# Kernel optimization log

Hardware: AMD Instinct MI355X
Metric: run time of the kernel (lower is better)

The kernel has to match this reference:

```python
import jax, jax.numpy as jnp
from jax import lax
import numpy as np

C, C_MID, K_ENC, K_UP, SCALE = 128, 64, 3, 5, 2
B, H, W = 4, 48, 48
BN_EPS = 1e-3  # ultralytics Conv BN eps
EPS = 1e-6


def setup_inputs() -> dict:
    key = jax.random.key(0)
    ks = jax.random.split(key, 12)
    n_enc = (SCALE * K_UP) ** 2  # 100
    return {
        "x": jax.random.uniform(ks[0], (B, C, H, W), dtype=jnp.float32),
        "comp_w": jax.random.normal(ks[1], (C_MID, C, 1, 1), dtype=jnp.float32) * 0.05,
        "comp_bn_g": jax.random.normal(ks[2], (C_MID,), dtype=jnp.float32) * 0.1 + 1.0,
        "comp_bn_b": jax.random.normal(ks[3], (C_MID,), dtype=jnp.float32) * 0.1,
        "comp_bn_m": jax.random.normal(ks[4], (C_MID,), dtype=jnp.float32) * 0.1,
        "comp_bn_v": jax.random.uniform(ks[5], (C_MID,), dtype=jnp.float32, minval=0.5, maxval=1.5),
        "enc_w": jax.random.normal(ks[6], (n_enc, C_MID, K_ENC, K_ENC), dtype=jnp.float32) * 0.05,
        "enc_bn_g": jax.random.normal(ks[7], (n_enc,), dtype=jnp.float32) * 0.1 + 1.0,
        "enc_bn_b": jax.random.normal(ks[8], (n_enc,), dtype=jnp.float32) * 0.1,
        "enc_bn_m": jax.random.normal(ks[9], (n_enc,), dtype=jnp.float32) * 0.1,
        "enc_bn_v": jax.random.uniform(ks[10], (n_enc,), dtype=jnp.float32, minval=0.5, maxval=1.5),
    }


def _conv_bn(x, w, g, b, m, v, pad, act):
    y = lax.conv_general_dilated(
        x, w, window_strides=(1, 1), padding=[(pad, pad), (pad, pad)],
        dimension_numbers=("NCHW", "OIHW", "NCHW"))
    scale = (g * lax.rsqrt(v + BN_EPS))[None, :, None, None]
    y = (y - m[None, :, None, None]) * scale + b[None, :, None, None]
    if act:  # SiLU
        y = y * jax.nn.sigmoid(y)
    return y


def reference(x, comp_w, comp_bn_g, comp_bn_b, comp_bn_m, comp_bn_v,
              enc_w, enc_bn_g, enc_bn_b, enc_bn_m, enc_bn_v):
    b, c, h, w = x.shape
    h_, w_ = h * SCALE, w * SCALE

    # ---- SAGamma: self-adaptive gamma correction ----
    gray = 0.299 * x[:, 0] + 0.587 * x[:, 1] + 0.114 * x[:, 2]  # (b,h,w)
    gm = jnp.mean(gray, axis=(1, 2), keepdims=True)              # (b,1,1)
    gs = jnp.std(gray, axis=(1, 2), ddof=1, keepdims=True)       # unbiased, like torch
    gamma = 0.8 + (1.2 - 0.8) * gm / (gm + jnp.maximum(gs, EPS))
    gamma = jnp.clip(gamma, 0.8, 1.2)[:, None]                   # (b,1,1,1)
    x = jnp.power(x + EPS, gamma)

    # ---- CARAFE ----
    # kernel prediction: comp (1x1 Conv+BN+SiLU) -> enc (3x3 Conv+BN, no act)
    Wk = _conv_bn(x, comp_w, comp_bn_g, comp_bn_b, comp_bn_m, comp_bn_v, pad=0, act=True)
    Wk = _conv_bn(Wk, enc_w, enc_bn_g, enc_bn_b, enc_bn_m, enc_bn_v, pad=K_ENC // 2, act=False)
    # pixel shuffle: (b, 25*s*s, h, w) -> (b, 25, h_, w_)
    k2 = K_UP * K_UP
    Wk = Wk.reshape(b, k2, SCALE, SCALE, h, w)
    Wk = Wk.transpose(0, 1, 4, 2, 5, 3).reshape(b, k2, h_, w_)
    Wk = jax.nn.softmax(Wk, axis=1)

    # nearest upsample x2
    Xu = jnp.repeat(jnp.repeat(x, SCALE, axis=2), SCALE, axis=3)  # (b,c,h_,w_)
    # unfold with kernel 5, dilation 2, pad 4 -> (b,c,25,h_,w_), torch (c,kh,kw) ordering
    pad = (K_UP // 2) * SCALE
    Xp = jnp.pad(Xu, ((0, 0), (0, 0), (pad, pad), (pad, pad)))
    patches = jnp.stack(
        [Xp[:, :, i * SCALE:i * SCALE + h_, j * SCALE:j * SCALE + w_]
         for i in range(K_UP) for j in range(K_UP)], axis=2)      # (b,c,25,h_,w_)

    return jnp.einsum("bkhw,bckhw->bchw", Wk, patches)
```

## Files before the change

kernel.cpp:

```cpp
#include <hip/hip_runtime.h>
#include <hip/hip_bf16.h>
#include <math.h>

#define CB   128
#define CMID 64
#define NENC 100
#define HH   48
#define WW   48
#define BB   4
#define HW   (HH*WW)
#define H2   (HH*2)
#define W2   (WW*2)
#define PS   56
#define PROWS 50
#define PCOL0 4
#define PLANE (PROWS*PS)
#define EG   2
#define NHALO4 (BB*CMID*124)

__global__ __launch_bounds__(256) void pow_kernel(const float* __restrict__ x,
                                                  float* __restrict__ xg,
                                                  float* __restrict__ y1p) {
    int tid = threadIdx.x;
    int bid = blockIdx.x;
    int b = bid / (CB * HW / 4 / 256);

    const float* xb = x + (size_t)b * CB * HW;
    const float4* R4 = (const float4*)xb;
    const float4* G4 = (const float4*)(xb + HW);
    const float4* B4 = (const float4*)(xb + 2 * HW);
    float s = 0.f, s2 = 0.f;
    for (int i = tid; i < HW / 4; i += 256) {
        float4 r = R4[i], g = G4[i], bl = B4[i];
        float g0 = 0.299f * r.x + 0.587f * g.x + 0.114f * bl.x;
        float g1 = 0.299f * r.y + 0.587f * g.y + 0.114f * bl.y;
        float g2 = 0.299f * r.z + 0.587f * g.z + 0.114f * bl.z;
        float g3 = 0.299f * r.w + 0.587f * g.w + 0.114f * bl.w;
        s  += (g0 + g1) + (g2 + g3);
        s2 += (g0 * g0 + g1 * g1) + (g2 * g2 + g3 * g3);
    }
    for (int o = 32; o > 0; o >>= 1) {
        s  += __shfl_down(s, o);
        s2 += __shfl_down(s2, o);
    }
    __shared__ float ss[4], ss2[4], gsh;
    int wid = tid >> 6;
    if ((tid & 63) == 0) { ss[wid] = s; ss2[wid] = s2; }
    __syncthreads();
    if (tid == 0) {
        float S = ss[0] + ss[1] + ss[2] + ss[3];
        float S2 = ss2[0] + ss2[1] + ss2[2] + ss2[3];
        const float N = (float)HW;
        float gm = S / N;
        float var = (S2 - S * S / N) / (N - 1.0f);
        var = fmaxf(var, 0.f);
        float gs = sqrtf(var);
        float gam = 0.8f + 0.4f * gm / (gm + fmaxf(gs, 1e-6f));
        gsh = fminf(fmaxf(gam, 0.8f), 1.2f);
    }
    __syncthreads();
    float gam = gsh;

    int idx = bid * 256 + tid;
    float4 xv = ((const float4*)x)[idx];
    float4 r;
    r.x = __expf(gam * __logf(xv.x + 1e-6f));
    r.y = __expf(gam * __logf(xv.y + 1e-6f));
    r.z = __expf(gam * __logf(xv.z + 1e-6f));
    r.w = __expf(gam * __logf(xv.w + 1e-6f));
    ((float4*)xg)[idx] = r;

    if (idx < NHALO4) {
        int plane = idx / 124;
        int t = idx % 124;
        float* p = y1p + (size_t)plane * PLANE;
        float4 z = make_float4(0.f, 0.f, 0.f, 0.f);
        if (t < 14) {
            *(float4*)(p + t * 4) = z;
        } else if (t < 28) {
            *(float4*)(p + 49 * PS + (t - 14) * 4) = z;
        } else {
            int sIdx = t - 28;
            int rr = 1 + (sIdx >> 1);
            int col = (sIdx & 1) ? 52 : 0;
            *(float4*)(p + rr * PS + col) = z;
        }
    }
}

__global__ void conv1_kernel(const float* __restrict__ xg, const float* __restrict__ w,
                             const float* __restrict__ g, const float* __restrict__ bta,
                             const float* __restrict__ m, const float* __restrict__ vv,
                             float* __restrict__ y1p) {
    int idx = blockIdx.x * blockDim.x + threadIdx.x;
    const int PG = HW / 4;
    const int total = BB * CMID * PG;
    if (idx >= total) return;
    int pg = idx % PG;
    int cm = (idx / PG) % CMID;
    int b  = idx / (CMID * PG);
    const float4* xb = (const float4*)(xg + (size_t)b * CB * HW) + pg;
    const float* wc = w + cm * CB;
    float4 acc = {0.f, 0.f, 0.f, 0.f};
#pragma unroll 8
    for (int c = 0; c < CB; c++) {
        float4 xv = xb[(size_t)c * PG];
        float wv = wc[c];
        acc.x = fmaf(wv, xv.x, acc.x);
        acc.y = fmaf(wv, xv.y, acc.y);
        acc.z = fmaf(wv, xv.z, acc.z);
        acc.w = fmaf(wv, xv.w, acc.w);
    }
    float sc = g[cm] * rsqrtf(vv[cm] + 1e-3f);
    float sh = bta[cm] - m[cm] * sc;
    float4 o;
    float t;
    t = acc.x * sc + sh; o.x = t / (1.f + __expf(-t));
    t = acc.y * sc + sh; o.y = t / (1.f + __expf(-t));
    t = acc.z * sc + sh; o.z = t / (1.f + __expf(-t));
    t = acc.w * sc + sh; o.w = t / (1.f + __expf(-t));
    int row = pg / 12, col = (pg % 12) * 4;
    float* dst = y1p + ((size_t)(b * CMID + cm)) * PLANE + (row + 1) * PS + (col + PCOL0);
    *(float4*)dst = o;
}

#define FMA4(A0,A1,A2,A3, wa,wb,wc, lf,mm,rt) \
    A0 = fmaf(wa, lf,   fmaf(wb, mm.x, fmaf(wc, mm.y, A0))); \
    A1 = fmaf(wa, mm.x, fmaf(wb, mm.y, fmaf(wc, mm.z, A1))); \
    A2 = fmaf(wa, mm.y, fmaf(wb, mm.z, fmaf(wc, mm.w, A2))); \
    A3 = fmaf(wa, mm.z, fmaf(wb, mm.w, fmaf(wc, rt,   A3)));

__global__ __launch_bounds__(192) void conv3_kernel(
        const float* __restrict__ y1p, const float* __restrict__ w,
        const float* __restrict__ g, const float* __restrict__ bta,
        const float* __restrict__ m, const float* __restrict__ vv,
        float* __restrict__ wk2n) {
    int blk = blockIdx.x;
    int eg  = blk % (NENC / EG);
    int tmp = blk / (NENC / EG);
    int rb  = tmp % 3, b = tmp / 3;
    int e0  = eg * EG;
    int t   = threadIdx.x;
    int row = rb * 16 + t / 12;
    int c0  = (t % 12) * 4;
    const float* wb0 = w + (size_t)e0 * CMID * 9;
    const float* wb1 = wb0 + CMID * 9;
    const float* yb = y1p + (size_t)b * CMID * PLANE + row * PS + (c0 + PCOL0);

    float a00 = 0.f, a01 = 0.f, a02 = 0.f, a03 = 0.f;
    float a10 = 0.f, a11 = 0.f, a12 = 0.f, a13 = 0.f;

    float  lf0 = yb[-1];        float4 m0 = *(const float4*)yb;          float rt0 = yb[4];
    float  lf1 = yb[PS-1];      float4 m1 = *(const float4*)(yb+PS);     float rt1 = yb[PS+4];
    float  lf2 = yb[2*PS-1];    float4 m2 = *(const float4*)(yb+2*PS);   float rt2 = yb[2*PS+4];
    float u00 = wb0[0], u01 = wb0[1], u02 = wb0[2];
    float u10 = wb0[3], u11 = wb0[4], u12 = wb0[5];
    float u20 = wb0[6], u21 = wb0[7], u22 = wb0[8];
    float v00 = wb1[0], v01 = wb1[1], v02 = wb1[2];
    float v10 = wb1[3], v11 = wb1[4], v12 = wb1[5];
    float v20 = wb1[6], v21 = wb1[7], v22 = wb1[8];

    for (int cm = 0; cm < CMID - 1; ++cm) {
        const float* yn = yb + (size_t)(cm + 1) * PLANE;
        float  nlf0 = yn[-1];       float4 nm0 = *(const float4*)yn;         float nrt0 = yn[4];
        float  nlf1 = yn[PS-1];     float4 nm1 = *(const float4*)(yn+PS);    float nrt1 = yn[PS+4];
        float  nlf2 = yn[2*PS-1];   float4 nm2 = *(const float4*)(yn+2*PS);  float nrt2 = yn[2*PS+4];
        const float* wn0 = wb0 + (cm + 1) * 9;
        const float* wn1 = wb1 + (cm + 1) * 9;
        float nu00 = wn0[0], nu01 = wn0[1], nu02 = wn0[2];
        float nu10 = wn0[3], nu11 = wn0[4], nu12 = wn0[5];
        float nu20 = wn0[6], nu21 = wn0[7], nu22 = wn0[8];
        float nv00 = wn1[0], nv01 = wn1[1], nv02 = wn1[2];
        float nv10 = wn1[3], nv11 = wn1[4], nv12 = wn1[5];
        float nv20 = wn1[6], nv21 = wn1[7], nv22 = wn1[8];

        FMA4(a00,a01,a02,a03, u00,u01,u02, lf0,m0,rt0)
        FMA4(a00,a01,a02,a03, u10,u11,u12, lf1,m1,rt1)
        FMA4(a00,a01,a02,a03, u20,u21,u22, lf2,m2,rt2)
        FMA4(a10,a11,a12,a13, v00,v01,v02, lf0,m0,rt0)
        FMA4(a10,a11,a12,a13, v10,v11,v12, lf1,m1,rt1)
        FMA4(a10,a11,a12,a13, v20,v21,v22, lf2,m2,rt2)

        lf0 = nlf0; m0 = nm0; rt0 = nrt0;
        lf1 = nlf1; m1 = nm1; rt1 = nrt1;
        lf2 = nlf2; m2 = nm2; rt2 = nrt2;
        u00 = nu00; u01 = nu01; u02 = nu02;
        u10 = nu10; u11 = nu11; u12 = nu12;
        u20 = nu20; u21 = nu21; u22 = nu22;
        v00 = nv00; v01 = nv01; v02 = nv02;
        v10 = nv10; v11 = nv11; v12 = nv12;
        v20 = nv20; v21 = nv21; v22 = nv22;
    }
    FMA4(a00,a01,a02,a03, u00,u01,u02, lf0,m0,rt0)
    FMA4(a00,a01,a02,a03, u10,u11,u12, lf1,m1,rt1)
    FMA4(a00,a01,a02,a03, u20,u21,u22, lf2,m2,rt2)
    FMA4(a10,a11,a12,a13, v00,v01,v02, lf0,m0,rt0)
    FMA4(a10,a11,a12,a13, v10,v11,v12, lf1,m1,rt1)
    FMA4(a10,a11,a12,a13, v20,v21,v22, lf2,m2,rt2)

    float sc0 = g[e0] * rsqrtf(vv[e0] + 1e-3f);
    float sh0 = bta[e0] - m[e0] * sc0;
    float sc1 = g[e0+1] * rsqrtf(vv[e0+1] + 1e-3f);
    float sh1 = bta[e0+1] - m[e0+1] * sc1;
    int kk = e0 >> 2, off0 = e0 & 3;
    float* op = wk2n + (((size_t)(b * 25 + kk) * HW + row * WW + c0) << 2) + off0;
    *(float2*)(op + 0)  = make_float2(a00*sc0+sh0, a10*sc1+sh1);
    *(float2*)(op + 4)  = make_float2(a01*sc0+sh0, a11*sc1+sh1);
    *(float2*)(op + 8)  = make_float2(a02*sc0+sh0, a12*sc1+sh1);
    *(float2*)(op + 12) = make_float2(a03*sc0+sh0, a13*sc1+sh1);
}

__global__ __launch_bounds__(256) void sg_kernel(const float* __restrict__ xg,
                                                 const float* __restrict__ wk2n,
                                                 float* __restrict__ out) {
    int blk = blockIdx.x;
    int whalf = blk & 1;
    int bh = blk >> 1;
    int h = bh % HH, b = bh / HH;
    int tid = threadIdx.x;

    __shared__ float raw[25 * 24 * 4];
    __shared__ float wsm[25 * 2 * 48];

    {
        const float4* w4p = (const float4*)wk2n;
        size_t base4 = (size_t)b * 25 * HW + h * WW + whalf * 24;
        float4* raw4 = (float4*)raw;
        for (int t = tid; t < 600; t += 256) {
            int k = t / 24, wl = t % 24;
            raw4[t] = w4p[base4 + (size_t)k * HW + wl];
        }
    }
    __syncthreads();
    if (tid < 96) {
        int wl = tid >> 2, off = tid & 3;
        float v[25]; float mx = -1e30f;
#pragma unroll
        for (int k = 0; k < 25; k++) { v[k] = raw[(k * 24 + wl) * 4 + off]; mx = fmaxf(mx, v[k]); }
        float sum = 0.f;
#pragma unroll
        for (int k = 0; k < 25; k++) { v[k] = __expf(v[k] - mx); sum += v[k]; }
        float inv = 1.f / sum;
        int si = off >> 1, sj = off & 1;
#pragma unroll
        for (int k = 0; k < 25; k++) wsm[k * 96 + si * 48 + 2 * wl + sj] = v[k] * inv;
    }
    __syncthreads();

    int c = tid >> 1, q = tid & 1;
    const float* xb = xg + ((size_t)b * CB + c) * HW;
    int wbase = whalf * 24 + q * 12;
    float* ob = out + (((size_t)b * CB + c) * H2 + 2 * h) * W2;
    const float4* wsm4 = (const float4*)wsm;
    const float4 Z4 = make_float4(0.f, 0.f, 0.f, 0.f);

    float4 A[5], Bv[5], Cv[5];
#pragma unroll
    for (int i = 0; i < 5; i++) {
        int hr = h + i - 2;
        bool rv = (hr >= 0) && (hr < HH);
        const float* rp = xb + hr * WW;
        A[i]  = (rv && wbase > 0) ? *(const float4*)(rp + wbase - 4) : Z4;
        Bv[i] = rv                ? *(const float4*)(rp + wbase)     : Z4;
        Cv[i] = rv                ? *(const float4*)(rp + wbase + 4) : Z4;
    }

#pragma unroll
    for (int s = 0; s < 3; s++) {
        int wc = wbase + 4 * s;
        float acc0[8], acc1[8];
#pragma unroll
        for (int p = 0; p < 8; p++) { acc0[p] = 0.f; acc1[p] = 0.f; }
#pragma unroll
        for (int i = 0; i < 5; i++) {
            float xv[12] = {A[i].x, A[i].y, A[i].z, A[i].w,
                            Bv[i].x, Bv[i].y, Bv[i].z, Bv[i].w,
                            Cv[i].x, Cv[i].y, Cv[i].z, Cv[i].w};
#pragma unroll
            for (int j = 0; j < 5; j++) {
                int k = i * 5 + j;
                float4 w0a = wsm4[k * 24 + 6 * q + 2 * s];
                float4 w0b = wsm4[k * 24 + 6 * q + 2 * s + 1];
                float4 w1a = wsm4[k * 24 + 12 + 6 * q + 2 * s];
                float4 w1b = wsm4[k * 24 + 12 + 6 * q + 2 * s + 1];
                float x0 = xv[j + 2], x1 = xv[j + 3], x2 = xv[j + 4], x3 = xv[j + 5];
                acc0[0] = fmaf(w0a.x, x0, acc0[0]); acc0[1] = fmaf(w0a.y, x0, acc0[1]);
                acc0[2] = fmaf(w0a.z, x1, acc0[2]); acc0[3] = fmaf(w0a.w, x1, acc0[3]);
                acc0[4] = fmaf(w0b.x, x2, acc0[4]); acc0[5] = fmaf(w0b.y, x2, acc0[5]);
                acc0[6] = fmaf(w0b.z, x3, acc0[6]); acc0[7] = fmaf(w0b.w, x3, acc0[7]);
                acc1[0] = fmaf(w1a.x, x0, acc1[0]); acc1[1] = fmaf(w1a.y, x0, acc1[1]);
                acc1[2] = fmaf(w1a.z, x1, acc1[2]); acc1[3] = fmaf(w1a.w, x1, acc1[3]);
                acc1[4] = fmaf(w1b.x, x2, acc1[4]); acc1[5] = fmaf(w1b.y, x2, acc1[5]);
                acc1[6] = fmaf(w1b.z, x3, acc1[6]); acc1[7] = fmaf(w1b.w, x3, acc1[7]);
            }
        }
        int colg = whalf * 48 + 24 * q + 8 * s;
        *(float4*)(ob + colg)          = make_float4(acc0[0], acc0[1], acc0[2], acc0[3]);
        *(float4*)(ob + colg + 4)      = make_float4(acc0[4], acc0[5], acc0[6], acc0[7]);
        *(float4*)(ob + W2 + colg)     = make_float4(acc1[0], acc1[1], acc1[2], acc1[3]);
        *(float4*)(ob + W2 + colg + 4) = make_float4(acc1[4], acc1[5], acc1[6], acc1[7]);
        if (s < 2) {
            int nc = wc + 8;
#pragma unroll
            for (int i = 0; i < 5; i++) {
                int hr = h + i - 2;
                bool rv = (hr >= 0) && (hr < HH);
                A[i] = Bv[i]; Bv[i] = Cv[i];
                Cv[i] = (rv && nc < WW) ? *(const float4*)(xb + hr * WW + nc) : Z4;
            }
        }
    }
}

extern "C" void kernel_launch(void* const* d_in, const int* in_sizes, int n_in,
                              void* d_out, int out_size, void* d_ws, size_t ws_size,
                              hipStream_t stream) {
    const float* x       = (const float*)d_in[0];
    const float* comp_w  = (const float*)d_in[1];
    const float* comp_g  = (const float*)d_in[2];
    const float* comp_b  = (const float*)d_in[3];
    const float* comp_m  = (const float*)d_in[4];
    const float* comp_v  = (const float*)d_in[5];
    const float* enc_w   = (const float*)d_in[6];
    const float* enc_g   = (const float*)d_in[7];
    const float* enc_b   = (const float*)d_in[8];
    const float* enc_m   = (const float*)d_in[9];
    const float* enc_v   = (const float*)d_in[10];
    float* out = (float*)d_out;

    float* ws = (float*)d_ws;
    float* xg    = ws;
    float* wk2n  = xg + (size_t)BB * CB * HW;
    float* y1p   = wk2n + (size_t)BB * 25 * HW * 4;

    {
        int total4 = BB * CB * HW / 4;
        pow_kernel<<<total4 / 256, 256, 0, stream>>>(x, xg, y1p);
    }
    {
        int total = BB * CMID * (HW / 4);
        conv1_kernel<<<(total + 255) / 256, 256, 0, stream>>>(
            xg, comp_w, comp_g, comp_b, comp_m, comp_v, y1p);
    }
    conv3_kernel<<<BB * 3 * (NENC / EG), 192, 0, stream>>>(
        y1p, enc_w, enc_g, enc_b, enc_m, enc_v, wk2n);
    sg_kernel<<<BB * HH * 2, 256, 0, stream>>>(xg, wk2n, out);
}
```

Baseline: 163.3 us.

## Split sg_kernel into narrower column segments and software-pipeline conv1 channel loads

The upsample/reassembly kernel now launches six blocks per row, each covering 8 input columns, instead of two blocks of 24. Each thread computes one output subrow of 16 values in a single pass, where before it made three sliding-window passes. This triples the grid to improve occupancy and latency hiding, at the cost of more redundant halo loads and a smaller softmax phase per block. Separately, conv1 prefetches the next 8 channels into registers while doing the FMAs on the current 8, and drops its bounds check because the thread count divides the grid exactly.

```diff
diff --git a/kernel.cpp b/kernel.cpp
--- a/kernel.cpp
+++ b/kernel.cpp
@@ -88,29 +88,49 @@
     }
 }
 
-__global__ void conv1_kernel(const float* __restrict__ xg, const float* __restrict__ w,
-                             const float* __restrict__ g, const float* __restrict__ bta,
-                             const float* __restrict__ m, const float* __restrict__ vv,
-                             float* __restrict__ y1p) {
-    int idx = blockIdx.x * blockDim.x + threadIdx.x;
+__global__ __launch_bounds__(256) void conv1_kernel(
+        const float* __restrict__ xg, const float* __restrict__ w,
+        const float* __restrict__ g, const float* __restrict__ bta,
+        const float* __restrict__ m, const float* __restrict__ vv,
+        float* __restrict__ y1p) {
+    int idx = blockIdx.x * 256 + threadIdx.x;
     const int PG = HW / 4;
-    const int total = BB * CMID * PG;
-    if (idx >= total) return;
     int pg = idx % PG;
     int cm = (idx / PG) % CMID;
     int b  = idx / (CMID * PG);
     const float4* xb = (const float4*)(xg + (size_t)b * CB * HW) + pg;
     const float* wc = w + cm * CB;
     float4 acc = {0.f, 0.f, 0.f, 0.f};
-#pragma unroll 8
-    for (int c = 0; c < CB; c++) {
-        float4 xv = xb[(size_t)c * PG];
-        float wv = wc[c];
-        acc.x = fmaf(wv, xv.x, acc.x);
-        acc.y = fmaf(wv, xv.y, acc.y);
-        acc.z = fmaf(wv, xv.z, acc.z);
-        acc.w = fmaf(wv, xv.w, acc.w);
-    }
+
+    float4 xr[8]; float wr[8];
+#pragma unroll
+    for (int j = 0; j < 8; j++) { xr[j] = xb[(size_t)j * PG]; wr[j] = wc[j]; }
+
+    for (int c = 0; c < CB - 8; c += 8) {
+        float4 nx[8]; float nw[8];
+#pragma unroll
+        for (int j = 0; j < 8; j++) {
+            nx[j] = xb[(size_t)(c + 8 + j) * PG];
+            nw[j] = wc[c + 8 + j];
+        }
+#pragma unroll
+        for (int j = 0; j < 8; j++) {
+            acc.x = fmaf(wr[j], xr[j].x, acc.x);
+            acc.y = fmaf(wr[j], xr[j].y, acc.y);
+            acc.z = fmaf(wr[j], xr[j].z, acc.z);
+            acc.w = fmaf(wr[j], xr[j].w, acc.w);
+        }
+#pragma unroll
+        for (int j = 0; j < 8; j++) { xr[j] = nx[j]; wr[j] = nw[j]; }
+    }
+#pragma unroll
+    for (int j = 0; j < 8; j++) {
+        acc.x = fmaf(wr[j], xr[j].x, acc.x);
+        acc.y = fmaf(wr[j], xr[j].y, acc.y);
+        acc.z = fmaf(wr[j], xr[j].z, acc.z);
+        acc.w = fmaf(wr[j], xr[j].w, acc.w);
+    }
+
     float sc = g[cm] * rsqrtf(vv[cm] + 1e-3f);
     float sh = bta[cm] - m[cm] * sc;
     float4 o;
@@ -214,102 +234,86 @@
                                                  const float* __restrict__ wk2n,
                                                  float* __restrict__ out) {
     int blk = blockIdx.x;
-    int whalf = blk & 1;
-    int bh = blk >> 1;
+    int wseg = blk % 6;
+    int bh = blk / 6;
     int h = bh % HH, b = bh / HH;
     int tid = threadIdx.x;
-
-    __shared__ float raw[25 * 24 * 4];
-    __shared__ float wsm[25 * 2 * 48];
-
-    {
-        const float4* w4p = (const float4*)wk2n;
-        size_t base4 = (size_t)b * 25 * HW + h * WW + whalf * 24;
-        float4* raw4 = (float4*)raw;
-        for (int t = tid; t < 600; t += 256) {
-            int k = t / 24, wl = t % 24;
-            raw4[t] = w4p[base4 + (size_t)k * HW + wl];
-        }
+    int c0 = wseg * 8;
+
+    __shared__ float raw[25 * 8 * 4];
+    __shared__ float wsm[25 * 2 * 16];
+
+    if (tid < 200) {
+        int k = tid / 8, wl = tid % 8;
+        ((float4*)raw)[tid] =
+            ((const float4*)wk2n)[((size_t)(b * 25 + k)) * HW + h * WW + c0 + wl];
     }
     __syncthreads();
-    if (tid < 96) {
+    if (tid < 32) {
         int wl = tid >> 2, off = tid & 3;
         float v[25]; float mx = -1e30f;
 #pragma unroll
-        for (int k = 0; k < 25; k++) { v[k] = raw[(k * 24 + wl) * 4 + off]; mx = fmaxf(mx, v[k]); }
+        for (int k = 0; k < 25; k++) { v[k] = raw[(k * 8 + wl) * 4 + off]; mx = fmaxf(mx, v[k]); }
         float sum = 0.f;
 #pragma unroll
         for (int k = 0; k < 25; k++) { v[k] = __expf(v[k] - mx); sum += v[k]; }
         float inv = 1.f / sum;
         int si = off >> 1, sj = off & 1;
 #pragma unroll
-        for (int k = 0; k < 25; k++) wsm[k * 96 + si * 48 + 2 * wl + sj] = v[k] * inv;
+        for (int k = 0; k < 25; k++) wsm[k * 32 + si * 16 + 2 * wl + sj] = v[k] * inv;
     }
     __syncthreads();
 
-    int c = tid >> 1, q = tid & 1;
+    int c = tid >> 1, si = tid & 1;
     const float* xb = xg + ((size_t)b * CB + c) * HW;
-    int wbase = whalf * 24 + q * 12;
-    float* ob = out + (((size_t)b * CB + c) * H2 + 2 * h) * W2;
     const float4* wsm4 = (const float4*)wsm;
     const float4 Z4 = make_float4(0.f, 0.f, 0.f, 0.f);
-
-    float4 A[5], Bv[5], Cv[5];
+    float acc[16];
+#pragma unroll
+    for (int t = 0; t < 16; t++) acc[t] = 0.f;
+
 #pragma unroll
     for (int i = 0; i < 5; i++) {
         int hr = h + i - 2;
         bool rv = (hr >= 0) && (hr < HH);
-        const float* rp = xb + hr * WW;
-        A[i]  = (rv && wbase > 0) ? *(const float4*)(rp + wbase - 4) : Z4;
-        Bv[i] = rv                ? *(const float4*)(rp + wbase)     : Z4;
-        Cv[i] = rv                ? *(const float4*)(rp + wbase + 4) : Z4;
-    }
-
-#pragma unroll
-    for (int s = 0; s < 3; s++) {
-        int wc = wbase + 4 * s;
-        float acc0[8], acc1[8];
-#pragma unroll
-        for (int p = 0; p < 8; p++) { acc0[p] = 0.f; acc1[p] = 0.f; }
-#pragma unroll
-        for (int i = 0; i < 5; i++) {
-            float xv[12] = {A[i].x, A[i].y, A[i].z, A[i].w,
-                            Bv[i].x, Bv[i].y, Bv[i].z, Bv[i].w,
-                            Cv[i].x, Cv[i].y, Cv[i].z, Cv[i].w};
-#pragma unroll
-            for (int j = 0; j < 5; j++) {
-                int k = i * 5 + j;
-                float4 w0a = wsm4[k * 24 + 6 * q + 2 * s];
-                float4 w0b = wsm4[k * 24 + 6 * q + 2 * s + 1];
-                float4 w1a = wsm4[k * 24 + 12 + 6 * q + 2 * s];
-                float4 w1b = wsm4[k * 24 + 12 + 6 * q + 2 * s + 1];
-                float x0 = xv[j + 2], x1 = xv[j + 3], x2 = xv[j + 4], x3 = xv[j + 5];
-                acc0[0] = fmaf(w0a.x, x0, acc0[0]); acc0[1] = fmaf(w0a.y, x0, acc0[1]);
-                acc0[2] = fmaf(w0a.z, x1, acc0[2]); acc0[3] = fmaf(w0a.w, x1, acc0[3]);
-                acc0[4] = fmaf(w0b.x, x2, acc0[4]); acc0[5] = fmaf(w0b.y, x2, acc0[5]);
-                acc0[6] = fmaf(w0b.z, x3, acc0[6]); acc0[7] = fmaf(w0b.w, x3, acc0[7]);
-                acc1[0] = fmaf(w1a.x, x0, acc1[0]); acc1[1] = fmaf(w1a.y, x0, acc1[1]);
-                acc1[2] = fmaf(w1a.z, x1, acc1[2]); acc1[3] = fmaf(w1a.w, x1, acc1[3]);
-                acc1[4] = fmaf(w1b.x, x2, acc1[4]); acc1[5] = fmaf(w1b.y, x2, acc1[5]);
-                acc1[6] = fmaf(w1b.z, x3, acc1[6]); acc1[7] = fmaf(w1b.w, x3, acc1[7]);
-            }
+        const float* rp = xb + hr * WW + c0;
+        float4 A  = (rv && wseg > 0) ? *(const float4*)(rp - 4) : Z4;
+        float4 Bq = rv               ? *(const float4*)(rp)     : Z4;
+        float4 Cq = rv               ? *(const float4*)(rp + 4) : Z4;
+        float4 D  = (rv && wseg < 5) ? *(const float4*)(rp + 8) : Z4;
+        float v[16] = {A.x, A.y, A.z, A.w, Bq.x, Bq.y, Bq.z, Bq.w,
+                       Cq.x, Cq.y, Cq.z, Cq.w, D.x, D.y, D.z, D.w};
+#pragma unroll
+        for (int j = 0; j < 5; j++) {
+            int k = i * 5 + j;
+            float4 wA = wsm4[k * 8 + si * 4 + 0];
+            float4 wB = wsm4[k * 8 + si * 4 + 1];
+            float4 wC = wsm4[k * 8 + si * 4 + 2];
+            float4 wD = wsm4[k * 8 + si * 4 + 3];
+            acc[0]  = fmaf(wA.x, v[j + 2], acc[0]);
+            acc[1]  = fmaf(wA.y, v[j + 2], acc[1]);
+            acc[2]  = fmaf(wA.z, v[j + 3], acc[2]);
+            acc[3]  = fmaf(wA.w, v[j + 3], acc[3]);
+            acc[4]  = fmaf(wB.x, v[j + 4], acc[4]);
+            acc[5]  = fmaf(wB.y, v[j + 4], acc[5]);
+            acc[6]  = fmaf(wB.z, v[j + 5], acc[6]);
+            acc[7]  = fmaf(wB.w, v[j + 5], acc[7]);
+            acc[8]  = fmaf(wC.x, v[j + 6], acc[8]);
+            acc[9]  = fmaf(wC.y, v[j + 6], acc[9]);
+            acc[10] = fmaf(wC.z, v[j + 7], acc[10]);
+            acc[11] = fmaf(wC.w, v[j + 7], acc[11]);
+            acc[12] = fmaf(wD.x, v[j + 8], acc[12]);
+            acc[13] = fmaf(wD.y, v[j + 8], acc[13]);
+            acc[14] = fmaf(wD.z, v[j + 9], acc[14]);
+            acc[15] = fmaf(wD.w, v[j + 9], acc[15]);
         }
-        int colg = whalf * 48 + 24 * q + 8 * s;
-        *(float4*)(ob + colg)          = make_float4(acc0[0], acc0[1], acc0[2], acc0[3]);
-        *(float4*)(ob + colg + 4)      = make_float4(acc0[4], acc0[5], acc0[6], acc0[7]);
-        *(float4*)(ob + W2 + colg)     = make_float4(acc1[0], acc1[1], acc1[2], acc1[3]);
-        *(float4*)(ob + W2 + colg + 4) = make_float4(acc1[4], acc1[5], acc1[6], acc1[7]);
-        if (s < 2) {
-            int nc = wc + 8;
-#pragma unroll
-            for (int i = 0; i < 5; i++) {
-                int hr = h + i - 2;
-                bool rv = (hr >= 0) && (hr < HH);
-                A[i] = Bv[i]; Bv[i] = Cv[i];
-                Cv[i] = (rv && nc < WW) ? *(const float4*)(xb + hr * WW + nc) : Z4;
-            }
-        }
-    }
+    }
+
+    float* ob = out + (((size_t)b * CB + c) * H2 + 2 * h + si) * W2 + 16 * wseg;
+    *(float4*)(ob + 0)  = make_float4(acc[0],  acc[1],  acc[2],  acc[3]);
+    *(float4*)(ob + 4)  = make_float4(acc[4],  acc[5],  acc[6],  acc[7]);
+    *(float4*)(ob + 8)  = make_float4(acc[8],  acc[9],  acc[10], acc[11]);
+    *(float4*)(ob + 12) = make_float4(acc[12], acc[13], acc[14], acc[15]);
 }
 
 extern "C" void kernel_launch(void* const* d_in, const int* in_sizes, int n_in,
@@ -339,10 +343,10 @@
     }
     {
         int total = BB * CMID * (HW / 4);
-        conv1_kernel<<<(total + 255) / 256, 256, 0, stream>>>(
+        conv1_kernel<<<total / 256, 256, 0, stream>>>(
             xg, comp_w, comp_g, comp_b, comp_m, comp_v, y1p);
     }
     conv3_kernel<<<BB * 3 * (NENC / EG), 192, 0, stream>>>(
         y1p, enc_w, enc_g, enc_b, enc_m, enc_v, wk2n);
-    sg_kernel<<<BB * HH * 2, 256, 0, stream>>>(xg, wk2n, out);
-}
+    sg_kernel<<<BB * HH * 6, 256, 0, stream>>>(xg, wk2n, out);
+}
```

New measurement: 176.2 us. 7.9% more time.
